# Kernel tuning notes

Measured on AMD Instinct MI355X. Metric: run time of the kernel, lower is better.

## Reference

```python
import jax, jax.numpy as jnp
import numpy as np

N_NODES = 50000
N_EDGES = 800000
HID = 256
OUT = 128
NEG_SLOPE = 0.2


def gat_layer(x, src, dst, W_src, W_dst, a_src_vec, a_dst_vec, bias, n_nodes):
    # Dense projections (PyG lin_src / lin_dst for tuple in_channels)
    h_src = x @ W_src              # [N, C]
    h_dst = x @ W_dst              # [N, C]
    # Per-node attention logits (att_src/att_dst dot products)
    a_src = h_src @ a_src_vec      # [N]
    a_dst = h_dst @ a_dst_vec      # [N]
    # Edge logits + LeakyReLU
    e = jax.nn.leaky_relu(a_src[src] + a_dst[dst], NEG_SLOPE)  # [E]
    # Segment softmax over incoming edges of each dst node
    m = jax.ops.segment_max(e, dst, num_segments=n_nodes)      # [N]
    m = jnp.where(jnp.isfinite(m), m, 0.0)                      # empty segments
    ex = jnp.exp(e - m[dst])                                    # [E]
    s = jax.ops.segment_sum(ex, dst, num_segments=n_nodes)     # [N]
    alpha = ex / (s[dst] + 1e-16)                               # [E]
    # Attention-weighted message aggregation (scatter-add to dst)
    msg = alpha[:, None] * h_src[src]                           # [E, C]
    out = jax.ops.segment_sum(msg, dst, num_segments=n_nodes)  # [N, C]
    return out + bias


def setup_inputs() -> dict:
    key = jax.random.key(0)
    ks = jax.random.split(key, 12)
    x = jax.random.normal(ks[0], (N_NODES, HID), dtype=jnp.float32)
    edge_index = jax.random.randint(ks[1], (2, N_EDGES), 0, N_NODES, dtype=jnp.int64)
    sc1 = 1.0 / np.sqrt(HID)
    sc2 = 1.0 / np.sqrt(HID)
    return {
        "x": x,
        "edge_index": edge_index,
        "W1_src": jax.random.normal(ks[2], (HID, HID), dtype=jnp.float32) * sc1,
        "W1_dst": jax.random.normal(ks[3], (HID, HID), dtype=jnp.float32) * sc1,
        "att1_src": jax.random.normal(ks[4], (HID,), dtype=jnp.float32) * sc1,
        "att1_dst": jax.random.normal(ks[5], (HID,), dtype=jnp.float32) * sc1,
        "b1": jnp.zeros((HID,), dtype=jnp.float32),
        "W2_src": jax.random.normal(ks[6], (HID, OUT), dtype=jnp.float32) * sc2,
        "W2_dst": jax.random.normal(ks[7], (HID, OUT), dtype=jnp.float32) * sc2,
        "att2_src": jax.random.normal(ks[8], (OUT,), dtype=jnp.float32) * (1.0 / np.sqrt(OUT)),
        "att2_dst": jax.random.normal(ks[9], (OUT,), dtype=jnp.float32) * (1.0 / np.sqrt(OUT)),
        "b2": jnp.zeros((OUT,), dtype=jnp.float32),
    }


def reference(x, edge_index, W1_src, W1_dst, att1_src, att1_dst, b1,
              W2_src, W2_dst, att2_src, att2_dst, b2):
    src, dst = edge_index[0], edge_index[1]
    h = gat_layer(x, src, dst, W1_src, W1_dst, att1_src, att1_dst, b1, N_NODES)
    h = jax.nn.relu(h)
    out = gat_layer(h, src, dst, W2_src, W2_dst, att2_src, att2_dst, b2, N_NODES)
    return out
```

## Files before the change

kernel.cpp:

```cpp
#include <hip/hip_runtime.h>
#include <math.h>

#define N_NODES 50000
#define N_EDGES 800000
#define HID 256
#define OUT_C 128
#define NEG_SLOPE 0.2f
#define SCAN_NB ((N_NODES + 255) / 256)

typedef __attribute__((ext_vector_type(8))) short bf16x8;
typedef __attribute__((ext_vector_type(4))) float f32x4;
typedef _Float16 half_t;
typedef __attribute__((ext_vector_type(4))) _Float16 half4;

__device__ inline unsigned short bf16_rne(float x) {
    unsigned u = __float_as_uint(x);
    return (unsigned short)((u + 0x7fffu + ((u >> 16) & 1u)) >> 16);
}


__global__ __launch_bounds__(256) void hist_rank_kernel(
    const int* __restrict__ dst, int* __restrict__ counts, int* __restrict__ rank) {
    int e = blockIdx.x * 256 + threadIdx.x;
    if (e < N_EDGES) rank[e] = atomicAdd(&counts[dst[e]], 1);
}

__global__ __launch_bounds__(256) void block_scan_kernel(
    const int* __restrict__ counts, int* __restrict__ excl,
    int* __restrict__ blockSums, int n) {
    __shared__ int waveSums[4];
    int i = blockIdx.x * 256 + threadIdx.x;
    int lane = threadIdx.x & 63;
    int wv = threadIdx.x >> 6;
    int c = (i < n) ? counts[i] : 0;
    int v = c;
    #pragma unroll
    for (int off = 1; off < 64; off <<= 1) {
        int t = __shfl_up(v, off);
        if (lane >= off) v += t;
    }
    if (lane == 63) waveSums[wv] = v;
    __syncthreads();
    int waveOff = 0;
    #pragma unroll
    for (int w = 0; w < 4; w++)
        if (w < wv) waveOff += waveSums[w];
    if (i < n) excl[i] = waveOff + v - c;
    if (threadIdx.x == 255) blockSums[blockIdx.x] = waveOff + v;
}

__global__ __launch_bounds__(256) void add_offsets_kernel(
    int* __restrict__ excl, const int* __restrict__ blockSums, int n) {
    __shared__ int lds[4];
    int tid = threadIdx.x;
    int partial = 0;
    for (int j = tid; j < (int)blockIdx.x; j += 256) partial += blockSums[j];
    #pragma unroll
    for (int off = 32; off > 0; off >>= 1) partial += __shfl_down(partial, off);
    if ((tid & 63) == 0) lds[tid >> 6] = partial;
    __syncthreads();
    int prefix = lds[0] + lds[1] + lds[2] + lds[3];
    int i = blockIdx.x * 256 + tid;
    if (i < n) excl[i] += prefix;
    if (i == 0) excl[n] = N_EDGES;
}


__global__ __launch_bounds__(256) void edge_weight_kernel(
    const int* __restrict__ src, const int* __restrict__ dst,
    const int* __restrict__ offsets, const int* __restrict__ rank,
    const float* __restrict__ a_src, const float* __restrict__ a_dst,
    int2* __restrict__ ew) {
    int e = blockIdx.x * 256 + threadIdx.x;
    if (e >= N_EDGES) return;
    int s = src[e], d = dst[e];
    float l = a_src[s] + a_dst[d];
    l = fmaxf(l, l * NEG_SLOPE);
    float w = __expf(l);
    ew[offsets[d] + rank[e]] = make_int2(s, __float_as_int(w));
}


__global__ __launch_bounds__(64) void compute_v_all_kernel(
    const float* __restrict__ W1s, const float* __restrict__ att1s,
    const float* __restrict__ W1d, const float* __restrict__ att1d,
    const float* __restrict__ W2s, const float* __restrict__ att2s,
    const float* __restrict__ W2d, const float* __restrict__ att2d,
    float* __restrict__ v1s, float* __restrict__ v1d,
    float* __restrict__ v2s, float* __restrict__ v2d) {
    int k = blockIdx.x;
    int lane = threadIdx.x;
    const float* W; const float* att; float* v; int cout;
    switch (blockIdx.y) {
        case 0: W = W1s; att = att1s; v = v1s; cout = HID; break;
        case 1: W = W1d; att = att1d; v = v1d; cout = HID; break;
        case 2: W = W2s; att = att2s; v = v2s; cout = OUT_C; break;
        default: W = W2d; att = att2d; v = v2d; cout = OUT_C; break;
    }
    float sum = 0.f;
    for (int j = lane; j < cout; j += 64)
        sum += W[k * cout + j] * att[j];
    #pragma unroll
    for (int off = 32; off > 0; off >>= 1)
        sum += __shfl_down(sum, off);
    if (lane == 0) v[k] = sum;
}


#define PACK1_T (8 * 17 * 64)
#define PACK2_T (8 * 9 * 64)

__global__ __launch_bounds__(256) void pack_all_kernel(
    const float* __restrict__ W1, const float* __restrict__ v1s, const float* __restrict__ v1d,
    const float* __restrict__ W2, const float* __restrict__ v2s, const float* __restrict__ v2d,
    unsigned short* __restrict__ hi1, unsigned short* __restrict__ lo1,
    unsigned short* __restrict__ hi2, unsigned short* __restrict__ lo2) {
    int t = blockIdx.x * 256 + threadIdx.x;
    const float *W, *vs, *vd; unsigned short *hi, *lo; int cout, NTL, tt;
    if (t < PACK1_T)            { tt = t;           W = W1; vs = v1s; vd = v1d; hi = hi1; lo = lo1; cout = HID;  NTL = 17; }
    else if (t < PACK1_T + PACK2_T) { tt = t - PACK1_T; W = W2; vs = v2s; vd = v2d; hi = hi2; lo = lo2; cout = OUT_C; NTL = 9; }
    else return;
    int lane = tt & 63;
    int tile = (tt >> 6) % NTL;
    int ks = tt / (64 * NTL);
    int m = lane & 15;
    int kbase = ks * 32 + (lane >> 4) * 8;
    #pragma unroll
    for (int j = 0; j < 8; j++) {
        float val;
        if (tile < NTL - 1) val = W[(kbase + j) * cout + tile * 16 + m];
        else val = (m == 0) ? vs[kbase + j] : (m == 1) ? vd[kbase + j] : 0.f;
        unsigned short h = bf16_rne(val);
        hi[tt * 8 + j] = h;
        lo[tt * 8 + j] = bf16_rne(val - __uint_as_float((unsigned)h << 16));
    }
}


template <int COUT, int NT, bool WRITE_A>
__device__ __forceinline__ void gemm_body(
    const float* __restrict__ A, const unsigned short* __restrict__ Bhi,
    const unsigned short* __restrict__ Blo, half_t* __restrict__ H,
    float* __restrict__ a_s, float* __restrict__ a_d, int M, int tile0) {
    const int NTL = COUT / 16 + 1;
    int wave = threadIdx.x >> 6, lane = threadIdx.x & 63;
    int m = lane & 15, quad = lane >> 4;
    int row0 = blockIdx.x * 128 + wave * 32;
    f32x4 acc[2][NT];
    #pragma unroll
    for (int rg = 0; rg < 2; rg++)
        #pragma unroll
        for (int nt = 0; nt < NT; nt++)
            acc[rg][nt] = (f32x4){0.f, 0.f, 0.f, 0.f};

    const float* arow[2];
    #pragma unroll
    for (int rg = 0; rg < 2; rg++) {
        int r = row0 + rg * 16 + m;
        if (r >= M) r = M - 1;
        arow[rg] = A + (size_t)r * HID;
    }

    for (int ks = 0; ks < 8; ks++) {
        bf16x8 ah[2], al[2];
        #pragma unroll
        for (int rg = 0; rg < 2; rg++) {
            const float* ap = arow[rg] + ks * 32 + quad * 8;
            float4 v0 = *(const float4*)ap;
            float4 v1 = *(const float4*)(ap + 4);
            float av[8] = {v0.x, v0.y, v0.z, v0.w, v1.x, v1.y, v1.z, v1.w};
            #pragma unroll
            for (int j = 0; j < 8; j++) {
                unsigned short h = bf16_rne(av[j]);
                float hf = __uint_as_float((unsigned)h << 16);
                ah[rg][j] = (short)h;
                al[rg][j] = (short)bf16_rne(av[j] - hf);
            }
        }
        #pragma unroll
        for (int nt = 0; nt < NT; nt++) {
            int tile = (WRITE_A && nt == NT - 1) ? (COUT / 16) : (tile0 + nt);
            size_t fbase = ((size_t)(ks * NTL + tile) * 64 + lane) * 8;
            bf16x8 bh = *(const bf16x8*)(Bhi + fbase);
            bf16x8 bl = *(const bf16x8*)(Blo + fbase);
            acc[0][nt] = __builtin_amdgcn_mfma_f32_16x16x32_bf16(ah[0], bh, acc[0][nt], 0, 0, 0);
            acc[1][nt] = __builtin_amdgcn_mfma_f32_16x16x32_bf16(ah[1], bh, acc[1][nt], 0, 0, 0);
            acc[0][nt] = __builtin_amdgcn_mfma_f32_16x16x32_bf16(ah[0], bl, acc[0][nt], 0, 0, 0);
            acc[1][nt] = __builtin_amdgcn_mfma_f32_16x16x32_bf16(ah[1], bl, acc[1][nt], 0, 0, 0);
            acc[0][nt] = __builtin_amdgcn_mfma_f32_16x16x32_bf16(al[0], bh, acc[0][nt], 0, 0, 0);
            acc[1][nt] = __builtin_amdgcn_mfma_f32_16x16x32_bf16(al[1], bh, acc[1][nt], 0, 0, 0);
        }
    }
    const int NW = WRITE_A ? NT - 1 : NT;
    #pragma unroll
    for (int rg = 0; rg < 2; rg++)
        #pragma unroll
        for (int nt = 0; nt < NW; nt++)
            #pragma unroll
            for (int r = 0; r < 4; r++) {
                int row = row0 + rg * 16 + quad * 4 + r;
                if (row < M)
                    H[(size_t)row * COUT + (tile0 + nt) * 16 + m] = (half_t)acc[rg][nt][r];
            }
    if (WRITE_A) {
        #pragma unroll
        for (int rg = 0; rg < 2; rg++)
            #pragma unroll
            for (int r = 0; r < 4; r++) {
                int row = row0 + rg * 16 + quad * 4 + r;
                if (row < M) {
                    if (m == 0) a_s[row] = acc[rg][NT - 1][r];
                    else if (m == 1) a_d[row] = acc[rg][NT - 1][r];
                }
            }
    }
}

template <int COUT>
__global__ __launch_bounds__(256) void mfma_gemm_a_kernel(
    const float* __restrict__ A, const unsigned short* __restrict__ Bhi,
    const unsigned short* __restrict__ Blo, half_t* __restrict__ H,
    float* __restrict__ a_s, float* __restrict__ a_d, int M) {
    if (blockIdx.y == 0)
        gemm_body<COUT, 9, true>(A, Bhi, Blo, H, a_s, a_d, M, 0);
    else
        gemm_body<COUT, 8, false>(A, Bhi, Blo, H, a_s, a_d, M, 8);
}


template <int C, bool RELU>
__global__ __launch_bounds__(256) void fused_aggregate_kernel(
    const int* __restrict__ offsets, const int2* __restrict__ ew,
    const half_t* __restrict__ h, const float* __restrict__ bias,
    float* __restrict__ out) {
    constexpr int CH = 16;
    constexpr int G = 8;
    constexpr int NPB = 32;
    int bx = blockIdx.x;
    int xcd = bx & 7;
    int nb = bx >> 3;
    int slice, nodeBase, nodeLim;
    if (C == 256) { slice = xcd; nodeBase = 0; nodeLim = N_NODES; }
    else { slice = xcd & 3; nodeBase = (xcd >> 2) * (N_NODES / 2); nodeLim = nodeBase + N_NODES / 2; }
    int wave = threadIdx.x >> 6, lane = threadIdx.x & 63;
    int sub = lane >> 3, gl = lane & 7;
    int node = nodeBase + nb * NPB + wave * 8 + sub;
    if (node >= nodeLim) return;
    int beg = offsets[node], end = offsets[node + 1];
    int c0 = slice * 32 + gl * 4;
    const half_t* hs = h + c0;
    float acc0 = 0.f, acc1 = 0.f, acc2 = 0.f, acc3 = 0.f, ssum = 0.f;

    for (int base = beg; base < end; base += CH) {
        int cnt = end - base; if (cnt > CH) cnt = CH;
        int2 ev0 = ew[base + ((gl < cnt) ? gl : 0)];
        int2 ev1 = ew[base + ((gl + 8 < cnt) ? gl + 8 : 0)];
        int idxs[CH]; float w[CH];
        #pragma unroll
        for (int j = 0; j < 8; j++) {
            idxs[j] = __shfl(ev0.x, j, G);
            float wv = __int_as_float(__shfl(ev0.y, j, G));
            w[j] = (j < cnt) ? wv : 0.f;
        }
        #pragma unroll
        for (int j = 0; j < 8; j++) {
            idxs[8 + j] = __shfl(ev1.x, j, G);
            float wv = __int_as_float(__shfl(ev1.y, j, G));
            w[8 + j] = (8 + j < cnt) ? wv : 0.f;
        }
        half4 hv[CH];
        #pragma unroll
        for (int j = 0; j < CH; j++)
            hv[j] = *(const half4*)(hs + (size_t)(unsigned)idxs[j] * C);
        #pragma unroll
        for (int j = 0; j < CH; j++) {
            ssum += w[j];
            acc0 += w[j] * (float)hv[j][0];
            acc1 += w[j] * (float)hv[j][1];
            acc2 += w[j] * (float)hv[j][2];
            acc3 += w[j] * (float)hv[j][3];
        }
    }

    float inv = 1.f / (ssum + 1e-16f);
    float4 bv = *(const float4*)(bias + c0);
    float o0 = acc0 * inv + bv.x, o1 = acc1 * inv + bv.y;
    float o2 = acc2 * inv + bv.z, o3 = acc3 * inv + bv.w;
    if (RELU) {
        o0 = fmaxf(o0, 0.f); o1 = fmaxf(o1, 0.f);
        o2 = fmaxf(o2, 0.f); o3 = fmaxf(o3, 0.f);
    }
    *(float4*)(out + (size_t)node * C + c0) = make_float4(o0, o1, o2, o3);
}

extern "C" void kernel_launch(void* const* d_in, const int* in_sizes, int n_in,
                              void* d_out, int out_size, void* d_ws, size_t ws_size,
                              hipStream_t stream) {
    const float* x     = (const float*)d_in[0];
    const int*   edge  = (const int*)d_in[1];
    const int*   src   = edge;
    const int*   dst   = edge + N_EDGES;
    const float* W1s   = (const float*)d_in[2];
    const float* W1d   = (const float*)d_in[3];
    const float* att1s = (const float*)d_in[4];
    const float* att1d = (const float*)d_in[5];
    const float* b1    = (const float*)d_in[6];
    const float* W2s   = (const float*)d_in[7];
    const float* W2d   = (const float*)d_in[8];
    const float* att2s = (const float*)d_in[9];
    const float* att2d = (const float*)d_in[10];
    const float* b2    = (const float*)d_in[11];
    float* out = (float*)d_out;

    float* ws    = (float*)d_ws;
    half_t* h1   = (half_t*)ws;
    int2* ew     = (int2*)(ws + (size_t)N_NODES * HID / 2);
    float* act2  = ws + (size_t)N_NODES * HID;
    float* a_s   = act2 + (size_t)N_NODES * HID;
    float* a_d   = a_s + N_NODES;
    float* vbuf  = a_d + N_NODES;
    int* ibase      = (int*)(vbuf + 4 * HID);
    int* rank       = ibase;
    int* counts     = rank + N_EDGES;
    int* offsets    = counts + N_NODES;
    int* blockSums  = offsets + N_NODES + 1;
    unsigned short* wp1h = (unsigned short*)(((uintptr_t)(blockSums + SCAN_NB) + 15) & ~(uintptr_t)15);
    unsigned short* wp1l = wp1h + PACK1_T * 8;
    unsigned short* wp2h = wp1l + PACK1_T * 8;
    unsigned short* wp2l = wp2h + PACK2_T * 8;
    float* v1s = vbuf, *v1d = vbuf + HID, *v2s = vbuf + 2 * HID, *v2d = vbuf + 3 * HID;
    half_t* h2 = h1;

    const int edgeBlocks = (N_EDGES + 255) / 256;
    const int gemmBlocks = (N_NODES + 127) / 128;
    const int aggBlocks1 = 8 * ((N_NODES + 31) / 32);
    const int aggBlocks2 = 8 * ((N_NODES / 2 + 31) / 32);

    hipMemsetAsync(counts, 0, N_NODES * sizeof(int), stream);
    hist_rank_kernel<<<edgeBlocks, 256, 0, stream>>>(dst, counts, rank);
    block_scan_kernel<<<SCAN_NB, 256, 0, stream>>>(counts, offsets, blockSums, N_NODES);
    add_offsets_kernel<<<SCAN_NB, 256, 0, stream>>>(offsets, blockSums, N_NODES);

    compute_v_all_kernel<<<dim3(HID, 4), 64, 0, stream>>>(
        W1s, att1s, W1d, att1d, W2s, att2s, W2d, att2d, v1s, v1d, v2s, v2d);
    pack_all_kernel<<<(PACK1_T + PACK2_T + 255) / 256, 256, 0, stream>>>(
        W1s, v1s, v1d, W2s, v2s, v2d, wp1h, wp1l, wp2h, wp2l);

    mfma_gemm_a_kernel<HID><<<dim3(gemmBlocks, 2), 256, 0, stream>>>(
        x, wp1h, wp1l, h1, a_s, a_d, N_NODES);
    edge_weight_kernel<<<edgeBlocks, 256, 0, stream>>>(
        src, dst, offsets, rank, a_s, a_d, ew);
    fused_aggregate_kernel<HID, true><<<aggBlocks1, 256, 0, stream>>>(
        offsets, ew, h1, b1, act2);

    mfma_gemm_a_kernel<OUT_C><<<dim3(gemmBlocks, 1), 256, 0, stream>>>(
        act2, wp2h, wp2l, h2, a_s, a_d, N_NODES);
    edge_weight_kernel<<<edgeBlocks, 256, 0, stream>>>(
        src, dst, offsets, rank, a_s, a_d, ew);
    fused_aggregate_kernel<OUT_C, false><<<aggBlocks2, 256, 0, stream>>>(
        offsets, ew, h2, b2, out);
}
```

Baseline: 376.8 us.

## Use persistent aggregation blocks with per-XCD atomic work queues and stealing

Replaces the static blockIdx-to-XCD mapping in the aggregation kernels with a fixed grid of persistent blocks. Each block reads its hardware XCC id and pulls node chunks from an atomic queue for its own channel slice, then steals from the other slices' queues once its own is empty. The goal is to keep each slice's feature columns resident in the local L2 even if the scheduler does not place blocks round-robin, and to balance uneven degree workloads. The cost is two block-wide barriers and an atomic per chunk, plus the queue counters that must be reset by a memset.

```diff
diff --git a/kernel.cpp b/kernel.cpp
--- a/kernel.cpp
+++ b/kernel.cpp
@@ -232,65 +232,80 @@
 __global__ __launch_bounds__(256) void fused_aggregate_kernel(
     const int* __restrict__ offsets, const int2* __restrict__ ew,
     const half_t* __restrict__ h, const float* __restrict__ bias,
-    float* __restrict__ out) {
+    float* __restrict__ out, int* __restrict__ qcur) {
     constexpr int CH = 16;
     constexpr int G = 8;
     constexpr int NPB = 32;
-    int bx = blockIdx.x;
-    int xcd = bx & 7;
-    int nb = bx >> 3;
-    int slice, nodeBase, nodeLim;
-    if (C == 256) { slice = xcd; nodeBase = 0; nodeLim = N_NODES; }
-    else { slice = xcd & 3; nodeBase = (xcd >> 2) * (N_NODES / 2); nodeLim = nodeBase + N_NODES / 2; }
+    constexpr int NSEG = (C == 256) ? N_NODES : N_NODES / 2;
+    constexpr int NCH = (NSEG + NPB - 1) / NPB;
+    __shared__ int sChunk;
+
+    unsigned xcc;
+    asm volatile("s_getreg_b32 %0, hwreg(HW_REG_XCC_ID)" : "=s"(xcc));
+    int xcd = (int)(xcc & 7u);
     int wave = threadIdx.x >> 6, lane = threadIdx.x & 63;
     int sub = lane >> 3, gl = lane & 7;
-    int node = nodeBase + nb * NPB + wave * 8 + sub;
-    if (node >= nodeLim) return;
-    int beg = offsets[node], end = offsets[node + 1];
-    int c0 = slice * 32 + gl * 4;
-    const half_t* hs = h + c0;
-    float acc0 = 0.f, acc1 = 0.f, acc2 = 0.f, acc3 = 0.f, ssum = 0.f;
-
-    for (int base = beg; base < end; base += CH) {
-        int cnt = end - base; if (cnt > CH) cnt = CH;
-        int2 ev0 = ew[base + ((gl < cnt) ? gl : 0)];
-        int2 ev1 = ew[base + ((gl + 8 < cnt) ? gl + 8 : 0)];
-        int idxs[CH]; float w[CH];
-        #pragma unroll
-        for (int j = 0; j < 8; j++) {
-            idxs[j] = __shfl(ev0.x, j, G);
-            float wv = __int_as_float(__shfl(ev0.y, j, G));
-            w[j] = (j < cnt) ? wv : 0.f;
+
+    for (int qi = 0; qi < 8; qi++) {
+        int qs = (xcd + qi) & 7;
+        int slice, nodeBase;
+        if (C == 256) { slice = qs; nodeBase = 0; }
+        else { slice = qs & 3; nodeBase = (qs >> 2) * (N_NODES / 2); }
+        int c0 = slice * 32 + gl * 4;
+        const half_t* hs = h + c0;
+        float4 bv = *(const float4*)(bias + c0);
+
+        while (true) {
+            __syncthreads();
+            if (threadIdx.x == 0) sChunk = atomicAdd(&qcur[qs], 1);
+            __syncthreads();
+            int chunk = sChunk;
+            if (chunk >= NCH) break;
+            int node = nodeBase + chunk * NPB + wave * 8 + sub;
+            if (node < nodeBase + NSEG) {
+                int beg = offsets[node], end = offsets[node + 1];
+                float acc0 = 0.f, acc1 = 0.f, acc2 = 0.f, acc3 = 0.f, ssum = 0.f;
+                for (int base = beg; base < end; base += CH) {
+                    int cnt = end - base; if (cnt > CH) cnt = CH;
+                    int2 ev0 = ew[base + ((gl < cnt) ? gl : 0)];
+                    int2 ev1 = ew[base + ((gl + 8 < cnt) ? gl + 8 : 0)];
+                    int idxs[CH]; float w[CH];
+                    #pragma unroll
+                    for (int j = 0; j < 8; j++) {
+                        idxs[j] = __shfl(ev0.x, j, G);
+                        float wv = __int_as_float(__shfl(ev0.y, j, G));
+                        w[j] = (j < cnt) ? wv : 0.f;
+                    }
+                    #pragma unroll
+                    for (int j = 0; j < 8; j++) {
+                        idxs[8 + j] = __shfl(ev1.x, j, G);
+                        float wv = __int_as_float(__shfl(ev1.y, j, G));
+                        w[8 + j] = (8 + j < cnt) ? wv : 0.f;
+                    }
+                    half4 hv[CH];
+                    #pragma unroll
+                    for (int j = 0; j < CH; j++)
+                        hv[j] = *(const half4*)(hs + (size_t)(unsigned)idxs[j] * C);
+                    #pragma unroll
+                    for (int j = 0; j < CH; j++) {
+                        ssum += w[j];
+                        acc0 += w[j] * (float)hv[j][0];
+                        acc1 += w[j] * (float)hv[j][1];
+                        acc2 += w[j] * (float)hv[j][2];
+                        acc3 += w[j] * (float)hv[j][3];
+                    }
+                }
+                float inv = 1.f / (ssum + 1e-16f);
+                float o0 = acc0 * inv + bv.x, o1 = acc1 * inv + bv.y;
+                float o2 = acc2 * inv + bv.z, o3 = acc3 * inv + bv.w;
+                if (RELU) {
+                    o0 = fmaxf(o0, 0.f); o1 = fmaxf(o1, 0.f);
+                    o2 = fmaxf(o2, 0.f); o3 = fmaxf(o3, 0.f);
+                }
+                *(float4*)(out + (size_t)node * C + c0) = make_float4(o0, o1, o2, o3);
+            }
         }
-        #pragma unroll
-        for (int j = 0; j < 8; j++) {
-            idxs[8 + j] = __shfl(ev1.x, j, G);
-            float wv = __int_as_float(__shfl(ev1.y, j, G));
-            w[8 + j] = (8 + j < cnt) ? wv : 0.f;
-        }
-        half4 hv[CH];
-        #pragma unroll
-        for (int j = 0; j < CH; j++)
-            hv[j] = *(const half4*)(hs + (size_t)(unsigned)idxs[j] * C);
-        #pragma unroll
-        for (int j = 0; j < CH; j++) {
-            ssum += w[j];
-            acc0 += w[j] * (float)hv[j][0];
-            acc1 += w[j] * (float)hv[j][1];
-            acc2 += w[j] * (float)hv[j][2];
-            acc3 += w[j] * (float)hv[j][3];
-        }
-    }
-
-    float inv = 1.f / (ssum + 1e-16f);
-    float4 bv = *(const float4*)(bias + c0);
-    float o0 = acc0 * inv + bv.x, o1 = acc1 * inv + bv.y;
-    float o2 = acc2 * inv + bv.z, o3 = acc3 * inv + bv.w;
-    if (RELU) {
-        o0 = fmaxf(o0, 0.f); o1 = fmaxf(o1, 0.f);
-        o2 = fmaxf(o2, 0.f); o3 = fmaxf(o3, 0.f);
-    }
-    *(float4*)(out + (size_t)node * C + c0) = make_float4(o0, o1, o2, o3);
+    }
 }
 
 extern "C" void kernel_launch(void* const* d_in, const int* in_sizes, int n_in,
@@ -324,7 +339,9 @@
     int* counts     = rank + N_EDGES;
     int* offsets    = counts + N_NODES;
     int* blockSums  = offsets + N_NODES + 1;
-    unsigned short* wp1h = (unsigned short*)(((uintptr_t)(blockSums + SCAN_NB) + 15) & ~(uintptr_t)15);
+    int* qA         = blockSums + SCAN_NB;
+    int* qB         = qA + 8;
+    unsigned short* wp1h = (unsigned short*)(((uintptr_t)(qB + 8) + 15) & ~(uintptr_t)15);
     unsigned short* wp1l = wp1h + PACK1_T * 8;
     unsigned short* wp2h = wp1l + PACK1_T * 8;
     unsigned short* wp2l = wp2h + PACK2_T * 8;
@@ -333,10 +350,10 @@
 
     const int edgeBlocks = (N_EDGES + 255) / 256;
     const int gemmBlocks = (N_NODES + 127) / 128;
-    const int aggBlocks1 = 8 * ((N_NODES + 31) / 32);
-    const int aggBlocks2 = 8 * ((N_NODES / 2 + 31) / 32);
+    const int aggBlocks = 2048;
 
     hipMemsetAsync(counts, 0, N_NODES * sizeof(int), stream);
+    hipMemsetAsync(qA, 0, 16 * sizeof(int), stream);
     hist_rank_kernel<<<edgeBlocks, 256, 0, stream>>>(dst, counts, rank);
     block_scan_kernel<<<SCAN_NB, 256, 0, stream>>>(counts, offsets, blockSums, N_NODES);
     add_offsets_kernel<<<SCAN_NB, 256, 0, stream>>>(offsets, blockSums, N_NODES);
@@ -350,13 +367,13 @@
         x, wp1h, wp1l, h1, a_s, a_d, N_NODES);
     edge_weight_kernel<<<edgeBlocks, 256, 0, stream>>>(
         src, dst, offsets, rank, a_s, a_d, ew);
-    fused_aggregate_kernel<HID, true><<<aggBlocks1, 256, 0, stream>>>(
-        offsets, ew, h1, b1, act2);
+    fused_aggregate_kernel<HID, true><<<aggBlocks, 256, 0, stream>>>(
+        offsets, ew, h1, b1, act2, qA);
 
     mfma_gemm_a_kernel<OUT_C><<<dim3(gemmBlocks, 1), 256, 0, stream>>>(
         act2, wp2h, wp2l, h2, a_s, a_d, N_NODES);
     edge_weight_kernel<<<edgeBlocks, 256, 0, stream>>>(
         src, dst, offsets, rank, a_s, a_d, ew);
-    fused_aggregate_kernel<OUT_C, false><<<aggBlocks2, 256, 0, stream>>>(
-        offsets, ew, h2, b2, out);
-}
+    fused_aggregate_kernel<OUT_C, false><<<aggBlocks, 256, 0, stream>>>(
+        offsets, ew, h2, b2, out, qB);
+}
```

Measured after the change: 783.2 us. +107.9%, slower.

## Store features in channel-sliced layout and aggregate one slice per launch

Applied to the files above, without the earlier changes.

The GEMM outputs and the layer-1 activations move to a sliced layout [slice][node][32], so each 32-channel slice of all nodes is contiguous. Each slice is then aggregated by its own sequential kernel launch, so a launch's gathered working set is one compact slice that can stay in L2/MALL. Before, the slice was chosen from XCD-interleaved block ids within a single launch. This adds 12 launches and their serialization in exchange for better gather locality. The second GEMM reads its activations from the sliced layout.

```diff
diff --git a/kernel.cpp b/kernel.cpp
--- a/kernel.cpp
+++ b/kernel.cpp
@@ -137,7 +137,7 @@
 }
 
 
-template <int COUT, int NT, bool WRITE_A>
+template <int COUT, int NT, bool WRITE_A, bool ASLICED>
 __device__ __forceinline__ void gemm_body(
     const float* __restrict__ A, const unsigned short* __restrict__ Bhi,
     const unsigned short* __restrict__ Blo, half_t* __restrict__ H,
@@ -158,14 +158,16 @@
     for (int rg = 0; rg < 2; rg++) {
         int r = row0 + rg * 16 + m;
         if (r >= M) r = M - 1;
-        arow[rg] = A + (size_t)r * HID;
+        arow[rg] = ASLICED ? (A + (size_t)r * 32) : (A + (size_t)r * HID);
     }
 
     for (int ks = 0; ks < 8; ks++) {
         bf16x8 ah[2], al[2];
         #pragma unroll
         for (int rg = 0; rg < 2; rg++) {
-            const float* ap = arow[rg] + ks * 32 + quad * 8;
+            const float* ap = ASLICED
+                ? (arow[rg] + (size_t)ks * N_NODES * 32 + quad * 8)
+                : (arow[rg] + ks * 32 + quad * 8);
             float4 v0 = *(const float4*)ap;
             float4 v1 = *(const float4*)(ap + 4);
             float av[8] = {v0.x, v0.y, v0.z, v0.w, v1.x, v1.y, v1.z, v1.w};
@@ -195,13 +197,17 @@
     #pragma unroll
     for (int rg = 0; rg < 2; rg++)
         #pragma unroll
-        for (int nt = 0; nt < NW; nt++)
+        for (int nt = 0; nt < NW; nt++) {
+            int t = tile0 + nt;
+            int sc = t >> 1;
+            int cc = (t & 1) * 16 + m;
             #pragma unroll
             for (int r = 0; r < 4; r++) {
                 int row = row0 + rg * 16 + quad * 4 + r;
                 if (row < M)
-                    H[(size_t)row * COUT + (tile0 + nt) * 16 + m] = (half_t)acc[rg][nt][r];
+                    H[((size_t)sc * N_NODES + row) * 32 + cc] = (half_t)acc[rg][nt][r];
             }
+        }
     if (WRITE_A) {
         #pragma unroll
         for (int rg = 0; rg < 2; rg++)
@@ -216,39 +222,32 @@
     }
 }
 
-template <int COUT>
+template <int COUT, bool ASLICED>
 __global__ __launch_bounds__(256) void mfma_gemm_a_kernel(
     const float* __restrict__ A, const unsigned short* __restrict__ Bhi,
     const unsigned short* __restrict__ Blo, half_t* __restrict__ H,
     float* __restrict__ a_s, float* __restrict__ a_d, int M) {
     if (blockIdx.y == 0)
-        gemm_body<COUT, 9, true>(A, Bhi, Blo, H, a_s, a_d, M, 0);
+        gemm_body<COUT, 9, true, ASLICED>(A, Bhi, Blo, H, a_s, a_d, M, 0);
     else
-        gemm_body<COUT, 8, false>(A, Bhi, Blo, H, a_s, a_d, M, 8);
-}
-
-
-template <int C, bool RELU>
-__global__ __launch_bounds__(256) void fused_aggregate_kernel(
+        gemm_body<COUT, 8, false, ASLICED>(A, Bhi, Blo, H, a_s, a_d, M, 8);
+}
+
+
+template <int C, bool RELU, bool OSLICED>
+__global__ __launch_bounds__(256) void fused_aggregate_slice_kernel(
     const int* __restrict__ offsets, const int2* __restrict__ ew,
     const half_t* __restrict__ h, const float* __restrict__ bias,
-    float* __restrict__ out) {
+    float* __restrict__ out, int slice) {
     constexpr int CH = 16;
     constexpr int G = 8;
-    constexpr int NPB = 32;
-    int bx = blockIdx.x;
-    int xcd = bx & 7;
-    int nb = bx >> 3;
-    int slice, nodeBase, nodeLim;
-    if (C == 256) { slice = xcd; nodeBase = 0; nodeLim = N_NODES; }
-    else { slice = xcd & 3; nodeBase = (xcd >> 2) * (N_NODES / 2); nodeLim = nodeBase + N_NODES / 2; }
     int wave = threadIdx.x >> 6, lane = threadIdx.x & 63;
     int sub = lane >> 3, gl = lane & 7;
-    int node = nodeBase + nb * NPB + wave * 8 + sub;
-    if (node >= nodeLim) return;
+    int node = blockIdx.x * 32 + wave * 8 + sub;
+    if (node >= N_NODES) return;
     int beg = offsets[node], end = offsets[node + 1];
     int c0 = slice * 32 + gl * 4;
-    const half_t* hs = h + c0;
+    const half_t* hs = h + (size_t)slice * N_NODES * 32 + gl * 4;
     float acc0 = 0.f, acc1 = 0.f, acc2 = 0.f, acc3 = 0.f, ssum = 0.f;
 
     for (int base = beg; base < end; base += CH) {
@@ -271,7 +270,7 @@
         half4 hv[CH];
         #pragma unroll
         for (int j = 0; j < CH; j++)
-            hv[j] = *(const half4*)(hs + (size_t)(unsigned)idxs[j] * C);
+            hv[j] = *(const half4*)(hs + (size_t)(unsigned)idxs[j] * 32);
         #pragma unroll
         for (int j = 0; j < CH; j++) {
             ssum += w[j];
@@ -290,7 +289,10 @@
         o0 = fmaxf(o0, 0.f); o1 = fmaxf(o1, 0.f);
         o2 = fmaxf(o2, 0.f); o3 = fmaxf(o3, 0.f);
     }
-    *(float4*)(out + (size_t)node * C + c0) = make_float4(o0, o1, o2, o3);
+    float* op = OSLICED
+        ? (out + ((size_t)slice * N_NODES + node) * 32 + gl * 4)
+        : (out + (size_t)node * C + c0);
+    *(float4*)op = make_float4(o0, o1, o2, o3);
 }
 
 extern "C" void kernel_launch(void* const* d_in, const int* in_sizes, int n_in,
@@ -333,8 +335,7 @@
 
     const int edgeBlocks = (N_EDGES + 255) / 256;
     const int gemmBlocks = (N_NODES + 127) / 128;
-    const int aggBlocks1 = 8 * ((N_NODES + 31) / 32);
-    const int aggBlocks2 = 8 * ((N_NODES / 2 + 31) / 32);
+    const int aggBlocks  = (N_NODES + 31) / 32;
 
     hipMemsetAsync(counts, 0, N_NODES * sizeof(int), stream);
     hist_rank_kernel<<<edgeBlocks, 256, 0, stream>>>(dst, counts, rank);
@@ -346,17 +347,19 @@
     pack_all_kernel<<<(PACK1_T + PACK2_T + 255) / 256, 256, 0, stream>>>(
         W1s, v1s, v1d, W2s, v2s, v2d, wp1h, wp1l, wp2h, wp2l);
 
-    mfma_gemm_a_kernel<HID><<<dim3(gemmBlocks, 2), 256, 0, stream>>>(
+    mfma_gemm_a_kernel<HID, false><<<dim3(gemmBlocks, 2), 256, 0, stream>>>(
         x, wp1h, wp1l, h1, a_s, a_d, N_NODES);
     edge_weight_kernel<<<edgeBlocks, 256, 0, stream>>>(
         src, dst, offsets, rank, a_s, a_d, ew);
-    fused_aggregate_kernel<HID, true><<<aggBlocks1, 256, 0, stream>>>(
-        offsets, ew, h1, b1, act2);
-
-    mfma_gemm_a_kernel<OUT_C><<<dim3(gemmBlocks, 1), 256, 0, stream>>>(
+    for (int s = 0; s < 8; s++)
+        fused_aggregate_slice_kernel<HID, true, true><<<aggBlocks, 256, 0, stream>>>(
+            offsets, ew, h1, b1, act2, s);
+
+    mfma_gemm_a_kernel<OUT_C, true><<<dim3(gemmBlocks, 1), 256, 0, stream>>>(
         act2, wp2h, wp2l, h2, a_s, a_d, N_NODES);
     edge_weight_kernel<<<edgeBlocks, 256, 0, stream>>>(
         src, dst, offsets, rank, a_s, a_d, ew);
-    fused_aggregate_kernel<OUT_C, false><<<aggBlocks2, 256, 0, stream>>>(
-        offsets, ew, h2, b2, out);
-}
+    for (int s = 0; s < 4; s++)
+        fused_aggregate_slice_kernel<OUT_C, false, false><<<aggBlocks, 256, 0, stream>>>(
+            offsets, ew, h2, b2, out, s);
+}
```

Result: slower. 405.0 us (+7.5%).
